# Optimization experiments

Measured on AMD Instinct MI355X. Metric: run time of the kernel, lower is better.

Reference implementation:

```python
import jax, jax.numpy as jnp
import numpy as np

TAU = 1.0
EPS = 1e-8  # F.cosine_similarity eps


def _cl(X, Y):
    # Pairwise cosine similarity via L2-normalize + single GEMM (N,D)@(D,N)
    Xn = X / jnp.maximum(jnp.linalg.norm(X, axis=1, keepdims=True), EPS)
    Yn = Y / jnp.maximum(jnp.linalg.norm(Y, axis=1, keepdims=True), EPS)
    sim = Xn @ Yn.T  # [N, N], sim[i, j] = cos(X_i, Y_j)
    e = jnp.exp(sim / TAU)
    pos = jnp.diagonal(e)               # exp(diag(sim)/tau), [N]
    neg = jnp.sum(e, axis=0) - pos      # column sums minus positive, [N]
    return -jnp.log(pos / neg).reshape(X.shape[0], 1)


def setup_inputs() -> dict:
    key = jax.random.key(0)
    ks = jax.random.split(key, 6)
    N, D1, D2, DO = 8192, 1024, 768, 256
    X = jax.random.normal(ks[0], (N, D1), dtype=jnp.float32)
    Y = jax.random.normal(ks[1], (N, D2), dtype=jnp.float32)
    # nn.Linear params (kaiming-uniform-ish scale)
    Wx = jax.random.uniform(ks[2], (DO, D1), jnp.float32, -1, 1) / np.sqrt(D1)
    bx = jax.random.uniform(ks[3], (DO,), jnp.float32, -1, 1) / np.sqrt(D1)
    Wy = jax.random.uniform(ks[4], (DO, D2), jnp.float32, -1, 1) / np.sqrt(D2)
    by = jax.random.uniform(ks[5], (DO,), jnp.float32, -1, 1) / np.sqrt(D2)
    return {"X": X, "Y": Y, "Wx": Wx, "bx": bx, "Wy": Wy, "by": by}


def reference(X, Y, Wx, bx, Wy, by):
    Xp = X @ Wx.T + bx  # proj_x
    Yp = Y @ Wy.T + by  # proj_y
    return _cl(Xp, Yp) + _cl(Yp, Xp)  # [N, 1]
```

## Files before the change

### kernel.cpp

```cpp
#include <hip/hip_runtime.h>
#include <hip/hip_bf16.h>

typedef __bf16 bf16_t;
typedef __bf16 bf16x4 __attribute__((ext_vector_type(4)));
typedef __bf16 bf16x8 __attribute__((ext_vector_type(8)));
typedef float  f32x4  __attribute__((ext_vector_type(4)));
typedef unsigned long u64;
typedef u64 u64x2 __attribute__((ext_vector_type(2)));

#if __has_builtin(__builtin_amdgcn_cvt_pk_fp8_f32)
__device__ __forceinline__ unsigned char cvt1_e4m3(float x) {
    return (unsigned char)(__builtin_amdgcn_cvt_pk_fp8_f32(x, x, 0, false) & 0xff);
}
#else
__device__ __forceinline__ unsigned char cvt1_e4m3(float x) {
    unsigned u = __float_as_uint(x);
    unsigned sign = (u >> 24) & 0x80u;
    float a = fabsf(x);
    if (a < 7.8125e-3f) { int q = (int)(a * 512.0f + 0.5f); return (unsigned char)(sign | q); }
    if (a >= 448.0f) return (unsigned char)(sign | 0x7E);
    unsigned au = u & 0x7FFFFFFFu;
    unsigned lsb = (au >> 20) & 1u;
    au += 0x7FFFFu + lsb;
    int exp = (int)(au >> 23) - 127;
    unsigned man = (au >> 20) & 7u;
    return (unsigned char)(sign | ((unsigned)(exp + 7) << 3) | man);
}
#endif

__device__ __forceinline__ int frag_off(int lr, int k) {
    return ((lr >> 4) << 12) + ((((k >> 6) << 2) + ((k >> 3) & 3)) << 8)
         + ((lr & 15) << 4) + (((k >> 5) & 1) << 3) + (k & 7);
}

__global__ __launch_bounds__(512) void proj_norm(
    const float* __restrict__ X, const float* __restrict__ Y,
    const float* __restrict__ Wxp, const float* __restrict__ bxp,
    const float* __restrict__ Wyp, const float* __restrict__ byp,
    unsigned char* __restrict__ Xt, unsigned char* __restrict__ Yt,
    float* __restrict__ sums)
{
    __shared__ bf16_t Abuf[64][40];
    __shared__ bf16_t Wbuf[256][40];
    __shared__ float  ssqL[4][64];
    __shared__ unsigned char obuf[16384];

    if (blockIdx.x < 32) sums[blockIdx.x * 512 + threadIdx.x] = 0.0f;

    const int tid  = threadIdx.x;
    const int lane = tid & 63;
    const int wave = tid >> 6;
    const int quad = lane >> 4;
    const int c16  = lane & 15;
    const int wy   = wave >> 2;
    const int wx   = wave & 3;

    const bool isY = blockIdx.x >= 128;
    const float* A    = isY ? Y   : X;
    const float* W    = isY ? Wyp : Wxp;
    const float* bias = isY ? byp : bxp;
    unsigned char* dst = isY ? Yt : Xt;
    const int K    = isY ? 768 : 1024;
    const int kit  = K >> 5;
    const int rowBase = (blockIdx.x & 127) * 64;

    const int sr = tid >> 3;
    const int sc = tid & 7;

    const float* pA = &A[(size_t)(rowBase + sr) * K + sc * 4];
    const float* pW = &W[(size_t)sr * K + sc * 4];

    f32x4 ra = *reinterpret_cast<const f32x4*>(pA);
    f32x4 rw[4];
    #pragma unroll
    for (int p = 0; p < 4; ++p)
        rw[p] = *reinterpret_cast<const f32x4*>(pW + (size_t)p * 64 * K);

    f32x4 acc[2][4] = {};

    for (int k = 0; k < kit; ++k) {
        __syncthreads();
        {
            bf16x4 h = { (bf16_t)ra.x, (bf16_t)ra.y, (bf16_t)ra.z, (bf16_t)ra.w };
            *reinterpret_cast<bf16x4*>(&Abuf[sr][sc * 4]) = h;
            #pragma unroll
            for (int p = 0; p < 4; ++p) {
                bf16x4 g = { (bf16_t)rw[p].x, (bf16_t)rw[p].y,
                             (bf16_t)rw[p].z, (bf16_t)rw[p].w };
                *reinterpret_cast<bf16x4*>(&Wbuf[p * 64 + sr][sc * 4]) = g;
            }
        }
        if (k + 1 < kit) {
            ra = *reinterpret_cast<const f32x4*>(pA + (k + 1) * 32);
            #pragma unroll
            for (int p = 0; p < 4; ++p)
                rw[p] = *reinterpret_cast<const f32x4*>(pW + (size_t)p * 64 * K + (k + 1) * 32);
        }
        __syncthreads();

        bf16x8 aF[2], bF[4];
        #pragma unroll
        for (int mf = 0; mf < 2; ++mf)
            aF[mf] = *reinterpret_cast<const bf16x8*>(&Abuf[wy * 32 + mf * 16 + c16][quad * 8]);
        #pragma unroll
        for (int nf = 0; nf < 4; ++nf)
            bF[nf] = *reinterpret_cast<const bf16x8*>(&Wbuf[wx * 64 + nf * 16 + c16][quad * 8]);
        #pragma unroll
        for (int mf = 0; mf < 2; ++mf)
            #pragma unroll
            for (int nf = 0; nf < 4; ++nf)
                acc[mf][nf] = __builtin_amdgcn_mfma_f32_16x16x32_bf16(
                    aF[mf], bF[nf], acc[mf][nf], 0, 0, 0);
    }

    #pragma unroll
    for (int nf = 0; nf < 4; ++nf) {
        float bb = bias[wx * 64 + nf * 16 + c16];
        #pragma unroll
        for (int mf = 0; mf < 2; ++mf)
            #pragma unroll
            for (int r = 0; r < 4; ++r)
                acc[mf][nf][r] += bb;
    }

    #pragma unroll
    for (int mf = 0; mf < 2; ++mf)
        #pragma unroll
        for (int r = 0; r < 4; ++r) {
            float v = 0.f;
            #pragma unroll
            for (int nf = 0; nf < 4; ++nf)
                v += acc[mf][nf][r] * acc[mf][nf][r];
            v += __shfl_xor(v, 1, 64);
            v += __shfl_xor(v, 2, 64);
            v += __shfl_xor(v, 4, 64);
            v += __shfl_xor(v, 8, 64);
            if (c16 == 0) ssqL[wx][wy * 32 + mf * 16 + quad * 4 + r] = v;
        }
    __syncthreads();

    #pragma unroll
    for (int mf = 0; mf < 2; ++mf)
        #pragma unroll
        for (int r = 0; r < 4; ++r) {
            int lr = wy * 32 + mf * 16 + quad * 4 + r;
            float t = ssqL[0][lr] + ssqL[1][lr] + ssqL[2][lr] + ssqL[3][lr];
            float inv = 1.0f / fmaxf(sqrtf(t), 1e-8f);
            #pragma unroll
            for (int nf = 0; nf < 4; ++nf) {
                int kcol = wx * 64 + nf * 16 + c16;
                obuf[frag_off(lr, kcol)] = cvt1_e4m3(acc[mf][nf][r] * inv);
            }
        }
    __syncthreads();

    {
        const f32x4* src = reinterpret_cast<const f32x4*>(&obuf[tid * 32]);
        f32x4* gout = reinterpret_cast<f32x4*>(dst + (size_t)rowBase * 256 + tid * 32);
        gout[0] = src[0];
        gout[1] = src[1];
    }
}

__global__ __launch_bounds__(256) void sim_gemm(
    const unsigned char* __restrict__ Xt, const unsigned char* __restrict__ Yt,
    float* __restrict__ rowsum, float* __restrict__ colsum,
    float* __restrict__ pos)
{
    __shared__ float red[256];

    const int tid  = threadIdx.x;
    const int lane = tid & 63;
    const int wave = tid >> 6;
    const int quad = lane >> 4;
    const int c16  = lane & 15;
    const int wy   = wave >> 1;
    const int wx   = wave & 1;
    const int rowBase = blockIdx.x * 128;
    const int colBase = blockIdx.y * 128;

    const u64x2* pa[4];
    const u64x2* pb[4];
    #pragma unroll
    for (int mf = 0; mf < 4; ++mf)
        pa[mf] = reinterpret_cast<const u64x2*>(
            Xt + (size_t)(rowBase + wy * 64 + mf * 16) * 256 + quad * 256 + c16 * 16);
    #pragma unroll
    for (int nf = 0; nf < 4; ++nf)
        pb[nf] = reinterpret_cast<const u64x2*>(
            Yt + (size_t)(colBase + wx * 64 + nf * 16) * 256 + quad * 256 + c16 * 16);

    f32x4 acc[4][4] = {};

    auto loadf = [&](u64x2* A, u64x2* B, int slab) {
        #pragma unroll
        for (int i = 0; i < 4; ++i) {
            A[i] = pa[i][slab * 64];
            B[i] = pb[i][slab * 64];
        }
    };
    auto mm = [&](const u64x2* A, const u64x2* B) {
        #pragma unroll
        for (int mf = 0; mf < 4; ++mf)
            #pragma unroll
            for (int nf = 0; nf < 4; ++nf)
                acc[mf][nf] = __builtin_amdgcn_mfma_f32_16x16x32_fp8_fp8(
                    (long)A[mf].x, (long)B[nf].x, acc[mf][nf], 0, 0, 0);
        #pragma unroll
        for (int mf = 0; mf < 4; ++mf)
            #pragma unroll
            for (int nf = 0; nf < 4; ++nf)
                acc[mf][nf] = __builtin_amdgcn_mfma_f32_16x16x32_fp8_fp8(
                    (long)A[mf].y, (long)B[nf].y, acc[mf][nf], 0, 0, 0);
    };

    u64x2 A0[4], B0[4], A1[4], B1[4];
    loadf(A0, B0, 0);
    loadf(A1, B1, 1);
    mm(A0, B0);
    loadf(A0, B0, 2);
    mm(A1, B1);
    loadf(A1, B1, 3);
    mm(A0, B0);
    mm(A1, B1);

    #pragma unroll
    for (int mf = 0; mf < 4; ++mf)
        #pragma unroll
        for (int nf = 0; nf < 4; ++nf)
            #pragma unroll
            for (int r = 0; r < 4; ++r)
                acc[mf][nf][r] = __expf(acc[mf][nf][r]);

    if (rowBase == colBase) {
        #pragma unroll
        for (int mf = 0; mf < 4; ++mf)
            #pragma unroll
            for (int nf = 0; nf < 4; ++nf)
                #pragma unroll
                for (int r = 0; r < 4; ++r) {
                    int lrow = wy * 64 + mf * 16 + quad * 4 + r;
                    int lcol = wx * 64 + nf * 16 + c16;
                    if (lrow == lcol) pos[rowBase + lrow] = acc[mf][nf][r];
                }
    }

    float rs[4][4];
    #pragma unroll
    for (int mf = 0; mf < 4; ++mf)
        #pragma unroll
        for (int r = 0; r < 4; ++r) {
            float v = acc[mf][0][r] + acc[mf][1][r] + acc[mf][2][r] + acc[mf][3][r];
            v += __shfl_xor(v, 1, 64);
            v += __shfl_xor(v, 2, 64);
            v += __shfl_xor(v, 4, 64);
            v += __shfl_xor(v, 8, 64);
            rs[mf][r] = v;
        }

    float cs[4];
    #pragma unroll
    for (int nf = 0; nf < 4; ++nf) {
        float v = 0.f;
        #pragma unroll
        for (int mf = 0; mf < 4; ++mf)
            #pragma unroll
            for (int r = 0; r < 4; ++r)
                v += acc[mf][nf][r];
        v += __shfl_xor(v, 16, 64);
        v += __shfl_xor(v, 32, 64);
        cs[nf] = v;
    }

    red[tid] = 0.f;
    __syncthreads();

    if (c16 == 0) {
        #pragma unroll
        for (int mf = 0; mf < 4; ++mf)
            #pragma unroll
            for (int r = 0; r < 4; ++r)
                atomicAdd(&red[wy * 64 + mf * 16 + quad * 4 + r], rs[mf][r]);
    }
    if (quad == 0) {
        #pragma unroll
        for (int nf = 0; nf < 4; ++nf)
            atomicAdd(&red[128 + wx * 64 + nf * 16 + c16], cs[nf]);
    }
    __syncthreads();

    if (tid < 128) atomicAdd(&rowsum[rowBase + tid], red[tid]);
    else           atomicAdd(&colsum[colBase + tid - 128], red[tid]);
}

__global__ __launch_bounds__(256) void finalize(
    const float* __restrict__ rowsum, const float* __restrict__ colsum,
    const float* __restrict__ pos, float* __restrict__ out)
{
    int i = blockIdx.x * 256 + threadIdx.x;
    float p = pos[i];
    out[i] = logf(colsum[i] - p) + logf(rowsum[i] - p) - 2.0f * logf(p);
}

extern "C" void kernel_launch(void* const* d_in, const int* in_sizes, int n_in,
                              void* d_out, int out_size, void* d_ws, size_t ws_size,
                              hipStream_t stream) {
    const float* X  = (const float*)d_in[0];
    const float* Y  = (const float*)d_in[1];
    const float* Wx = (const float*)d_in[2];
    const float* bx = (const float*)d_in[3];
    const float* Wy = (const float*)d_in[4];
    const float* by = (const float*)d_in[5];
    float* out = (float*)d_out;

    char* ws = (char*)d_ws;
    unsigned char* Xt = (unsigned char*)(ws);
    unsigned char* Yt = (unsigned char*)(ws + (2u << 20));
    float*  rowsum = (float*)(ws + (4u << 20));
    float*  colsum = rowsum + 8192;
    float*  pos    = colsum + 8192;

    proj_norm<<<256, 512, 0, stream>>>(X, Y, Wx, bx, Wy, by, Xt, Yt, rowsum);
    sim_gemm<<<dim3(64, 64), 256, 0, stream>>>(Xt, Yt, rowsum, colsum, pos);
    finalize<<<32, 256, 0, stream>>>(rowsum, colsum, pos, out);
}
```

Baseline: 168.2 us.

## Pre-convert weights to bf16 fragment layout and drop LDS staging in projection

Adds a wconv kernel that converts Wx/Wy to bf16 in MFMA fragment order and zeroes the sums. proj_norm is rewritten to read A and the weights straight from global memory into registers with double buffering, dropping the LDS staging and per-step barriers, and now uses 32-row blocks with 512 blocks. sim_gemm moves to 512 threads covering 256 rows per block, and the diagonal check is generalized. This trades an extra launch and higher register pressure for removing the LDS round trips and redundant weight conversion in the projection.

```diff
diff --git a/kernel.cpp b/kernel.cpp
--- a/kernel.cpp
+++ b/kernel.cpp
@@ -2,11 +2,16 @@
 #include <hip/hip_bf16.h>
 
 typedef __bf16 bf16_t;
-typedef __bf16 bf16x4 __attribute__((ext_vector_type(4)));
 typedef __bf16 bf16x8 __attribute__((ext_vector_type(8)));
 typedef float  f32x4  __attribute__((ext_vector_type(4)));
 typedef unsigned long u64;
 typedef u64 u64x2 __attribute__((ext_vector_type(2)));
+
+__device__ __forceinline__ bf16x8 pack8(f32x4 a, f32x4 b) {
+    bf16x8 h = { (bf16_t)a.x, (bf16_t)a.y, (bf16_t)a.z, (bf16_t)a.w,
+                 (bf16_t)b.x, (bf16_t)b.y, (bf16_t)b.z, (bf16_t)b.w };
+    return h;
+}
 
 #if __has_builtin(__builtin_amdgcn_cvt_pk_fp8_f32)
 __device__ __forceinline__ unsigned char cvt1_e4m3(float x) {
@@ -28,146 +33,151 @@
 }
 #endif
 
-__device__ __forceinline__ int frag_off(int lr, int k) {
-    return ((lr >> 4) << 12) + ((((k >> 6) << 2) + ((k >> 3) & 3)) << 8)
-         + ((lr & 15) << 4) + (((k >> 5) & 1) << 3) + (k & 7);
-}
-
-__global__ __launch_bounds__(512) void proj_norm(
-    const float* __restrict__ X, const float* __restrict__ Y,
-    const float* __restrict__ Wxp, const float* __restrict__ bxp,
-    const float* __restrict__ Wyp, const float* __restrict__ byp,
-    unsigned char* __restrict__ Xt, unsigned char* __restrict__ Yt,
+__device__ __forceinline__ int frag_off_k(int row16, int k) {
+    return ((k >> 6) << 10) + (((k >> 3) & 3) << 8) + (row16 << 4)
+         + (((k >> 5) & 1) << 3) + (k & 7);
+}
+
+__global__ __launch_bounds__(256) void wconv(
+    const float* __restrict__ Wx, const float* __restrict__ Wy,
+    bf16_t* __restrict__ Wxt, bf16_t* __restrict__ Wyt,
     float* __restrict__ sums)
 {
-    __shared__ bf16_t Abuf[64][40];
-    __shared__ bf16_t Wbuf[256][40];
-    __shared__ float  ssqL[4][64];
-    __shared__ unsigned char obuf[16384];
-
-    if (blockIdx.x < 32) sums[blockIdx.x * 512 + threadIdx.x] = 0.0f;
-
-    const int tid  = threadIdx.x;
-    const int lane = tid & 63;
-    const int wave = tid >> 6;
-    const int quad = lane >> 4;
-    const int c16  = lane & 15;
-    const int wy   = wave >> 2;
-    const int wx   = wave & 3;
-
-    const bool isY = blockIdx.x >= 128;
-    const float* A    = isY ? Y   : X;
-    const float* W    = isY ? Wyp : Wxp;
-    const float* bias = isY ? byp : bxp;
-    unsigned char* dst = isY ? Yt : Xt;
-    const int K    = isY ? 768 : 1024;
-    const int kit  = K >> 5;
-    const int rowBase = (blockIdx.x & 127) * 64;
-
-    const int sr = tid >> 3;
-    const int sc = tid & 7;
-
-    const float* pA = &A[(size_t)(rowBase + sr) * K + sc * 4];
-    const float* pW = &W[(size_t)sr * K + sc * 4];
-
-    f32x4 ra = *reinterpret_cast<const f32x4*>(pA);
-    f32x4 rw[4];
-    #pragma unroll
-    for (int p = 0; p < 4; ++p)
-        rw[p] = *reinterpret_cast<const f32x4*>(pW + (size_t)p * 64 * K);
-
-    f32x4 acc[2][4] = {};
-
-    for (int k = 0; k < kit; ++k) {
-        __syncthreads();
-        {
-            bf16x4 h = { (bf16_t)ra.x, (bf16_t)ra.y, (bf16_t)ra.z, (bf16_t)ra.w };
-            *reinterpret_cast<bf16x4*>(&Abuf[sr][sc * 4]) = h;
-            #pragma unroll
-            for (int p = 0; p < 4; ++p) {
-                bf16x4 g = { (bf16_t)rw[p].x, (bf16_t)rw[p].y,
-                             (bf16_t)rw[p].z, (bf16_t)rw[p].w };
-                *reinterpret_cast<bf16x4*>(&Wbuf[p * 64 + sr][sc * 4]) = g;
-            }
+    int id = blockIdx.x * 256 + threadIdx.x;
+    if (blockIdx.x < 64) sums[id] = 0.0f;
+
+    int row, k0, K;
+    const float* W;
+    bf16_t* Wt;
+    if (id < 32768) { W = Wx; Wt = Wxt; K = 1024; row = id >> 7; k0 = (id & 127) << 3; }
+    else { int c = id - 32768; W = Wy; Wt = Wyt; K = 768; row = c / 96; k0 = (c % 96) << 3; }
+
+    f32x4 lo = *reinterpret_cast<const f32x4*>(&W[(size_t)row * K + k0]);
+    f32x4 hi = *reinterpret_cast<const f32x4*>(&W[(size_t)row * K + k0 + 4]);
+    size_t off = (size_t)(row >> 4) * 16 * K + frag_off_k(row & 15, k0);
+    *reinterpret_cast<bf16x8*>(Wt + off) = pack8(lo, hi);
+}
+
+__global__ __launch_bounds__(256) void proj_norm(
+    const float* __restrict__ X, const float* __restrict__ Y,
+    const bf16_t* __restrict__ Wxt, const float* __restrict__ bxp,
+    const bf16_t* __restrict__ Wyt, const float* __restrict__ byp,
+    unsigned char* __restrict__ Xt, unsigned char* __restrict__ Yt)
+{
+    __shared__ unsigned char obuf[8192];
+    __shared__ float ssq2[2][2][16];
+
+    const int tid   = threadIdx.x;
+    const int lane  = tid & 63;
+    const int wave  = tid >> 6;
+    const int quad  = lane >> 4;
+    const int c16   = lane & 15;
+    const int strip = wave >> 1;
+    const int half  = wave & 1;
+
+    const bool isY = blockIdx.x >= 256;
+    const float*  A    = isY ? Y   : X;
+    const bf16_t* Wt   = isY ? Wyt : Wxt;
+    const float*  bias = isY ? byp : bxp;
+    unsigned char* dst = isY ? Yt  : Xt;
+    const int K = isY ? 768 : 1024;
+    const int S = K >> 6;
+    const int rowBase = (blockIdx.x & 255) * 32;
+    const int grow = rowBase + strip * 16 + c16;
+
+    const float*  pA = A + (size_t)grow * K + quad * 8;
+    const bf16_t* pB = Wt + (size_t)(half * 8) * 16 * K + quad * 256 + c16 * 16;
+    const size_t tStride = (size_t)16 * K;
+
+    f32x4  av0[4], av1[4];
+    bf16x8 bv0[8][2], bv1[8][2];
+    f32x4  acc[8] = {};
+
+    auto loadA = [&](f32x4* av, int s) {
+        const float* q = pA + s * 64;
+        av[0] = *reinterpret_cast<const f32x4*>(q);
+        av[1] = *reinterpret_cast<const f32x4*>(q + 4);
+        av[2] = *reinterpret_cast<const f32x4*>(q + 32);
+        av[3] = *reinterpret_cast<const f32x4*>(q + 36);
+    };
+    auto loadB = [&](bf16x8 (*bv)[2], int s) {
+        #pragma unroll
+        for (int nf = 0; nf < 8; ++nf) {
+            const bf16_t* p = pB + (size_t)nf * tStride + s * 1024;
+            bv[nf][0] = *reinterpret_cast<const bf16x8*>(p);
+            bv[nf][1] = *reinterpret_cast<const bf16x8*>(p + 8);
         }
-        if (k + 1 < kit) {
-            ra = *reinterpret_cast<const f32x4*>(pA + (k + 1) * 32);
-            #pragma unroll
-            for (int p = 0; p < 4; ++p)
-                rw[p] = *reinterpret_cast<const f32x4*>(pW + (size_t)p * 64 * K + (k + 1) * 32);
+    };
+    auto step = [&](const f32x4* av, const bf16x8 (*bv)[2]) {
+        bf16x8 aF0 = pack8(av[0], av[1]);
+        bf16x8 aF1 = pack8(av[2], av[3]);
+        #pragma unroll
+        for (int nf = 0; nf < 8; ++nf)
+            acc[nf] = __builtin_amdgcn_mfma_f32_16x16x32_bf16(aF0, bv[nf][0], acc[nf], 0, 0, 0);
+        #pragma unroll
+        for (int nf = 0; nf < 8; ++nf)
+            acc[nf] = __builtin_amdgcn_mfma_f32_16x16x32_bf16(aF1, bv[nf][1], acc[nf], 0, 0, 0);
+    };
+
+    loadA(av0, 0);
+    loadB(bv0, 0);
+    for (int s = 0; s < S; s += 2) {
+        if (s + 1 < S) { loadA(av1, s + 1); loadB(bv1, s + 1); }
+        step(av0, bv0);
+        if (s + 2 < S) { loadA(av0, s + 2); loadB(bv0, s + 2); }
+        step(av1, bv1);
+    }
+
+    #pragma unroll
+    for (int nf = 0; nf < 8; ++nf) {
+        float bb = bias[half * 128 + nf * 16 + c16];
+        #pragma unroll
+        for (int r = 0; r < 4; ++r) acc[nf][r] += bb;
+    }
+
+    float s4[4];
+    #pragma unroll
+    for (int r = 0; r < 4; ++r) {
+        float v = 0.f;
+        #pragma unroll
+        for (int nf = 0; nf < 8; ++nf) v += acc[nf][r] * acc[nf][r];
+        v += __shfl_xor(v, 1, 64);
+        v += __shfl_xor(v, 2, 64);
+        v += __shfl_xor(v, 4, 64);
+        v += __shfl_xor(v, 8, 64);
+        s4[r] = v;
+    }
+    if (c16 == 0) {
+        #pragma unroll
+        for (int r = 0; r < 4; ++r) ssq2[strip][half][quad * 4 + r] = s4[r];
+    }
+    __syncthreads();
+
+    #pragma unroll
+    for (int r = 0; r < 4; ++r) {
+        int row16 = quad * 4 + r;
+        float t = ssq2[strip][0][row16] + ssq2[strip][1][row16];
+        float inv = 1.0f / fmaxf(sqrtf(t), 1e-8f);
+        #pragma unroll
+        for (int nf = 0; nf < 8; ++nf) {
+            int k = half * 128 + nf * 16 + c16;
+            obuf[strip * 4096 + frag_off_k(row16, k)] = cvt1_e4m3(acc[nf][r] * inv);
         }
-        __syncthreads();
-
-        bf16x8 aF[2], bF[4];
-        #pragma unroll
-        for (int mf = 0; mf < 2; ++mf)
-            aF[mf] = *reinterpret_cast<const bf16x8*>(&Abuf[wy * 32 + mf * 16 + c16][quad * 8]);
-        #pragma unroll
-        for (int nf = 0; nf < 4; ++nf)
-            bF[nf] = *reinterpret_cast<const bf16x8*>(&Wbuf[wx * 64 + nf * 16 + c16][quad * 8]);
-        #pragma unroll
-        for (int mf = 0; mf < 2; ++mf)
-            #pragma unroll
-            for (int nf = 0; nf < 4; ++nf)
-                acc[mf][nf] = __builtin_amdgcn_mfma_f32_16x16x32_bf16(
-                    aF[mf], bF[nf], acc[mf][nf], 0, 0, 0);
-    }
-
-    #pragma unroll
-    for (int nf = 0; nf < 4; ++nf) {
-        float bb = bias[wx * 64 + nf * 16 + c16];
-        #pragma unroll
-        for (int mf = 0; mf < 2; ++mf)
-            #pragma unroll
-            for (int r = 0; r < 4; ++r)
-                acc[mf][nf][r] += bb;
-    }
-
-    #pragma unroll
-    for (int mf = 0; mf < 2; ++mf)
-        #pragma unroll
-        for (int r = 0; r < 4; ++r) {
-            float v = 0.f;
-            #pragma unroll
-            for (int nf = 0; nf < 4; ++nf)
-                v += acc[mf][nf][r] * acc[mf][nf][r];
-            v += __shfl_xor(v, 1, 64);
-            v += __shfl_xor(v, 2, 64);
-            v += __shfl_xor(v, 4, 64);
-            v += __shfl_xor(v, 8, 64);
-            if (c16 == 0) ssqL[wx][wy * 32 + mf * 16 + quad * 4 + r] = v;
-        }
+    }
     __syncthreads();
 
-    #pragma unroll
-    for (int mf = 0; mf < 2; ++mf)
-        #pragma unroll
-        for (int r = 0; r < 4; ++r) {
-            int lr = wy * 32 + mf * 16 + quad * 4 + r;
-            float t = ssqL[0][lr] + ssqL[1][lr] + ssqL[2][lr] + ssqL[3][lr];
-            float inv = 1.0f / fmaxf(sqrtf(t), 1e-8f);
-            #pragma unroll
-            for (int nf = 0; nf < 4; ++nf) {
-                int kcol = wx * 64 + nf * 16 + c16;
-                obuf[frag_off(lr, kcol)] = cvt1_e4m3(acc[mf][nf][r] * inv);
-            }
-        }
-    __syncthreads();
-
-    {
-        const f32x4* src = reinterpret_cast<const f32x4*>(&obuf[tid * 32]);
-        f32x4* gout = reinterpret_cast<f32x4*>(dst + (size_t)rowBase * 256 + tid * 32);
-        gout[0] = src[0];
-        gout[1] = src[1];
-    }
-}
-
-__global__ __launch_bounds__(256) void sim_gemm(
+    const f32x4* src = reinterpret_cast<const f32x4*>(&obuf[tid * 32]);
+    f32x4* g = reinterpret_cast<f32x4*>(dst + (size_t)rowBase * 256 + tid * 32);
+    g[0] = src[0];
+    g[1] = src[1];
+}
+
+__global__ __launch_bounds__(512) void sim_gemm(
     const unsigned char* __restrict__ Xt, const unsigned char* __restrict__ Yt,
     float* __restrict__ rowsum, float* __restrict__ colsum,
     float* __restrict__ pos)
 {
-    __shared__ float red[256];
+    __shared__ float red[384];
 
     const int tid  = threadIdx.x;
     const int lane = tid & 63;
@@ -176,7 +186,7 @@
     const int c16  = lane & 15;
     const int wy   = wave >> 1;
     const int wx   = wave & 1;
-    const int rowBase = blockIdx.x * 128;
+    const int rowBase = blockIdx.x * 256;
     const int colBase = blockIdx.y * 128;
 
     const u64x2* pa[4];
@@ -232,18 +242,16 @@
             for (int r = 0; r < 4; ++r)
                 acc[mf][nf][r] = __expf(acc[mf][nf][r]);
 
-    if (rowBase == colBase) {
-        #pragma unroll
-        for (int mf = 0; mf < 4; ++mf)
-            #pragma unroll
-            for (int nf = 0; nf < 4; ++nf)
-                #pragma unroll
-                for (int r = 0; r < 4; ++r) {
-                    int lrow = wy * 64 + mf * 16 + quad * 4 + r;
-                    int lcol = wx * 64 + nf * 16 + c16;
-                    if (lrow == lcol) pos[rowBase + lrow] = acc[mf][nf][r];
-                }
-    }
+    #pragma unroll
+    for (int mf = 0; mf < 4; ++mf)
+        #pragma unroll
+        for (int nf = 0; nf < 4; ++nf)
+            #pragma unroll
+            for (int r = 0; r < 4; ++r) {
+                int grow = rowBase + wy * 64 + mf * 16 + quad * 4 + r;
+                int gcol = colBase + wx * 64 + nf * 16 + c16;
+                if (grow == gcol) pos[grow] = acc[mf][nf][r];
+            }
 
     float rs[4][4];
     #pragma unroll
@@ -272,7 +280,7 @@
         cs[nf] = v;
     }
 
-    red[tid] = 0.f;
+    if (tid < 384) red[tid] = 0.f;
     __syncthreads();
 
     if (c16 == 0) {
@@ -285,12 +293,12 @@
     if (quad == 0) {
         #pragma unroll
         for (int nf = 0; nf < 4; ++nf)
-            atomicAdd(&red[128 + wx * 64 + nf * 16 + c16], cs[nf]);
+            atomicAdd(&red[256 + wx * 64 + nf * 16 + c16], cs[nf]);
     }
     __syncthreads();
 
-    if (tid < 128) atomicAdd(&rowsum[rowBase + tid], red[tid]);
-    else           atomicAdd(&colsum[colBase + tid - 128], red[tid]);
+    if (tid < 256)      atomicAdd(&rowsum[rowBase + tid], red[tid]);
+    else if (tid < 384) atomicAdd(&colsum[colBase + tid - 256], red[tid]);
 }
 
 __global__ __launch_bounds__(256) void finalize(
@@ -314,13 +322,16 @@
     float* out = (float*)d_out;
 
     char* ws = (char*)d_ws;
-    unsigned char* Xt = (unsigned char*)(ws);
-    unsigned char* Yt = (unsigned char*)(ws + (2u << 20));
-    float*  rowsum = (float*)(ws + (4u << 20));
-    float*  colsum = rowsum + 8192;
-    float*  pos    = colsum + 8192;
-
-    proj_norm<<<256, 512, 0, stream>>>(X, Y, Wx, bx, Wy, by, Xt, Yt, rowsum);
-    sim_gemm<<<dim3(64, 64), 256, 0, stream>>>(Xt, Yt, rowsum, colsum, pos);
+    unsigned char* Xt  = (unsigned char*)(ws);
+    unsigned char* Yt  = (unsigned char*)(ws + (2u << 20));
+    bf16_t*        Wxt = (bf16_t*)(ws + (4u << 20));
+    bf16_t*        Wyt = (bf16_t*)(ws + (4u << 20) + (512u << 10));
+    float* rowsum = (float*)(ws + (5u << 20));
+    float* colsum = rowsum + 8192;
+    float* pos    = colsum + 8192;
+
+    wconv<<<224, 256, 0, stream>>>(Wx, Wy, Wxt, Wyt, rowsum);
+    proj_norm<<<512, 256, 0, stream>>>(X, Y, Wxt, bx, Wyt, by, Xt, Yt);
+    sim_gemm<<<dim3(32, 64), 512, 0, stream>>>(Xt, Yt, rowsum, colsum, pos);
     finalize<<<32, 256, 0, stream>>>(rowsum, colsum, pos, out);
 }
```

Result: slower. 195.9 us (+16.5%).
